# Kernel tuning notes

Measured on AMD Instinct MI355X. Metric: run time of the kernel, lower is better.

The kernel has to match this reference:

```python
import jax, jax.numpy as jnp
import numpy as np

HIDDEN, HEAD_DIM, B, S = 1024, 64, 8, 2048


def setup_inputs() -> dict:
    key = jax.random.key(0)
    ks = jax.random.split(key, 8)
    scale = 1.0 / np.sqrt(HIDDEN)
    return {
        "query": jax.random.normal(ks[0], (B, S, HIDDEN), jnp.float32),
        "key": jax.random.normal(ks[1], (B, S, HIDDEN), jnp.float32),
        "value": jax.random.normal(ks[2], (B, S, HIDDEN), jnp.float32),
        "relative_biases": jax.random.normal(ks[3], (B, S, S), jnp.float32),
        "mask": jnp.ones((B, S), jnp.int32),
        "Wq": jax.random.normal(ks[4], (HEAD_DIM, HIDDEN), jnp.float32) * scale,
        "bq": jnp.zeros((HEAD_DIM,), jnp.float32),
        "Wk": jax.random.normal(ks[5], (HEAD_DIM, HIDDEN), jnp.float32) * scale,
        "bk": jnp.zeros((HEAD_DIM,), jnp.float32),
        "Wv": jax.random.normal(ks[6], (HEAD_DIM, HIDDEN), jnp.float32) * scale,
        "bv": jnp.zeros((HEAD_DIM,), jnp.float32),
    }


def reference(query, key, value, relative_biases, mask, Wq, bq, Wk, bk, Wv, bv):
    # Per-head linear projections: [B,S,H] @ [H,D] + [D]
    q = jnp.einsum("bsh,dh->bsd", query, Wq) + bq
    k = jnp.einsum("bsh,dh->bsd", key, Wk) + bk
    v = jnp.einsum("bsh,dh->bsd", value, Wv) + bv
    d = q.shape[-1]
    # (QK^T + relative_bias) / sqrt(d)  -- bias added BEFORE scaling, as in source
    scores = (jnp.einsum("bqd,bkd->bqk", q, k) + relative_biases) / jnp.sqrt(
        jnp.asarray(d, q.dtype)
    )
    # 2-D mask [B,Sk] broadcast over queries; masked_fill(mask==0, -inf)
    m = mask[:, None, :]  # [B,1,Sk]
    scores = jnp.where(m == 0, -jnp.inf, scores)
    att = jax.nn.softmax(scores, axis=-1)
    # dropout prob 0.0 (eval / identity)
    return jnp.einsum("bqk,bkd->bqd", att, v)
```

## Files before the change

### kernel.cpp

```cpp
#include <hip/hip_runtime.h>
#include <stdint.h>

typedef __bf16 bf16x4 __attribute__((ext_vector_type(4)));
typedef __bf16 bf16x8 __attribute__((ext_vector_type(8)));
typedef float  f32x4  __attribute__((ext_vector_type(4)));

#define HID 1024
#define SEQ 2048
#define NB  8

__device__ __forceinline__ void gl_lds16(const void* g, void* l) {
    __builtin_amdgcn_global_load_lds(
        (const __attribute__((address_space(1))) void*)g,
        (__attribute__((address_space(3))) void*)l, 16, 0, 0);
}

__global__ __launch_bounds__(256) void prep_w(
    const float* __restrict__ Wq, const float* __restrict__ Wk,
    const float* __restrict__ Wv, __bf16* __restrict__ Wb)
{
    const int i = blockIdx.x * 256 + threadIdx.x;
    const int mat = i >> 14;
    const int j   = i & 16383;
    const float* src = ((mat == 0) ? Wq : (mat == 1) ? Wk : Wv) + j * 4;
    float4 f = *(const float4*)src;
    bf16x4 o = { (__bf16)f.x, (__bf16)f.y, (__bf16)f.z, (__bf16)f.w };
    *(bf16x4*)(Wb + (size_t)i * 4) = o;
}

__global__ __launch_bounds__(256, 3) void proj_kernel(
    const float* __restrict__ Xq, const float* __restrict__ Xk, const float* __restrict__ Xv,
    const __bf16* __restrict__ Wb,
    const float* __restrict__ bq_, const float* __restrict__ bk_, const float* __restrict__ bv_,
    __bf16* __restrict__ qo, __bf16* __restrict__ ko, __bf16* __restrict__ vTo)
{
    const int mat = blockIdx.y;
    const float* X   = (mat == 0) ? Xq  : (mat == 1) ? Xk  : Xv;
    const __bf16* Wm = Wb + (size_t)mat * 64 * HID;
    const float* Bp  = (mat == 0) ? bq_ : (mat == 1) ? bk_ : bv_;

    const int row0 = blockIdx.x * 64;
    const int tid  = threadIdx.x;
    const int lane = tid & 63;
    const int wv   = tid >> 6;
    const int lr   = lane & 15;
    const int g    = lane >> 4;

    __shared__ __align__(16) float  Xl[2][64 * 64];
    __shared__ __align__(16) __bf16 Wl[2][64 * 64];

    f32x4 acc[4] = {};

    auto STAGE = [&](int t, int pb) {
        const int k0 = t * 64;
        #pragma unroll
        for (int j = 0; j < 4; ++j) {
            const int row = wv * 16 + 4 * j + (lane >> 4);
            const int c   = row & 7;
            const float* src = X + (size_t)(row0 + row) * HID + k0 + 4 * ((lane & 15) ^ c);
            gl_lds16(src, &Xl[pb][(wv * 16 + 4 * j) * 64]);
        }
        #pragma unroll
        for (int j = 0; j < 2; ++j) {
            const int row = wv * 16 + 8 * j + (lane >> 3);
            const int c   = row & 7;
            const __bf16* src = Wm + (size_t)row * HID + k0 + 8 * ((lane & 7) ^ c);
            gl_lds16(src, &Wl[pb][(wv * 16 + 8 * j) * 64]);
        }
    };

    STAGE(0, 0);
    STAGE(1, 1);

    const int r  = wv * 16 + lr;
    const int cx = lr & 7;

    for (int t = 0; t < 16; ++t) {
        const int pb = t & 1;
        if (t < 15) { asm volatile("s_waitcnt vmcnt(6)" ::: "memory"); }
        else        { asm volatile("s_waitcnt vmcnt(0)" ::: "memory"); }
        __builtin_amdgcn_s_barrier();

        #pragma unroll
        for (int kk = 0; kk < 2; ++kk) {
            const int ulo = 2 * g + 8 * kk;
            f32x4 xa = *(const f32x4*)&Xl[pb][r * 64 + (((ulo)     ^ cx) << 2)];
            f32x4 xb = *(const f32x4*)&Xl[pb][r * 64 + (((ulo + 1) ^ cx) << 2)];
            bf16x8 af = { (__bf16)xa.x, (__bf16)xa.y, (__bf16)xa.z, (__bf16)xa.w,
                          (__bf16)xb.x, (__bf16)xb.y, (__bf16)xb.z, (__bf16)xb.w };
            #pragma unroll
            for (int ct = 0; ct < 4; ++ct) {
                const int uw = g + 4 * kk;
                bf16x8 bf = *(const bf16x8*)&Wl[pb][(ct * 16 + lr) * 64 + ((uw ^ cx) << 3)];
                acc[ct] = __builtin_amdgcn_mfma_f32_16x16x32_bf16(af, bf, acc[ct], 0, 0, 0);
            }
        }

        __builtin_amdgcn_s_barrier();
        if (t + 2 < 16) STAGE(t + 2, pb);
    }

    const float scl = (mat == 0) ? 0.125f : 1.0f;
    float res[4][4];
    #pragma unroll
    for (int ct = 0; ct < 4; ++ct) {
        const float bval = Bp[ct * 16 + lr];
        #pragma unroll
        for (int rr = 0; rr < 4; ++rr) res[ct][rr] = (acc[ct][rr] + bval) * scl;
    }

    if (mat < 2) {
        __bf16* o = (mat == 0) ? qo : ko;
        #pragma unroll
        for (int ct = 0; ct < 4; ++ct)
            #pragma unroll
            for (int rr = 0; rr < 4; ++rr)
                o[(size_t)(row0 + wv * 16 + 4 * g + rr) * 64 + ct * 16 + lr] = (__bf16)res[ct][rr];
    } else {
        __bf16* Tl = (__bf16*)&Xl[0][0];
        __syncthreads();
        #pragma unroll
        for (int ct = 0; ct < 4; ++ct)
            #pragma unroll
            for (int rr = 0; rr < 4; ++rr)
                Tl[(ct * 16 + lr) * 72 + wv * 16 + 4 * g + rr] = (__bf16)res[ct][rr];
        __syncthreads();
        const int d   = tid >> 2;
        const int sc_ = (tid & 3) * 16;
        const int b   = row0 >> 11;
        const int s0  = row0 & 2047;
        __bf16* dst = vTo + ((size_t)b * 64 + d) * SEQ + s0 + sc_;
        *(bf16x8*)dst       = *(const bf16x8*)&Tl[d * 72 + sc_];
        *(bf16x8*)(dst + 8) = *(const bf16x8*)&Tl[d * 72 + sc_ + 8];
    }
}

__global__ __launch_bounds__(128) void attn_kernel(
    const __bf16* __restrict__ qws, const __bf16* __restrict__ kws,
    const __bf16* __restrict__ vTws, const float* __restrict__ bias,
    const int* __restrict__ mask, float* __restrict__ out)
{
    const int bid = blockIdx.x;
    const int b   = bid & 7;
    const int q0  = (bid >> 3) * 32;
    const int tid = threadIdx.x;
    const int lane = tid & 63;
    const int wv   = tid >> 6;
    const int lr   = lane & 15;
    const int g    = lane >> 4;

    __shared__ __align__(16) __bf16 Kl[64 * 72];
    __shared__ __align__(16) __bf16 Vl[64 * 72];

    const int qrow = q0 + wv * 16 + lr;

    bf16x8 qf[2];
    {
        const __bf16* qp = qws + (size_t)(b * SEQ + qrow) * 64;
        #pragma unroll
        for (int dt = 0; dt < 2; ++dt) {
            bf16x4 lo = *(const bf16x4*)(qp + dt * 32 + 4 * g);
            bf16x4 hi = *(const bf16x4*)(qp + dt * 32 + 16 + 4 * g);
            qf[dt] = __builtin_shufflevector(lo, hi, 0, 1, 2, 3, 4, 5, 6, 7);
        }
    }

    f32x4 O[4] = {};
    float m   = -3.0e38f;
    float ell = 0.0f;

    const float* brow = bias + (size_t)(b * SEQ + qrow) * SEQ;
    const int*   mrow = mask + b * SEQ;

    const int sr = tid >> 1;
    const int sc = (tid & 1) * 32;
    const __bf16* kbase = kws  + (size_t)(b * SEQ + sr) * 64 + sc;
    const __bf16* vbase = vTws + ((size_t)b * 64 + sr) * SEQ + sc;

    bf16x8 kr[4], vr[4];
    float4 bvn[4]; int4 mkn[4];

    auto loadt = [&](int kt) {
        const __bf16* ks = kbase + (size_t)kt * 64;
        kr[0] = *(const bf16x8*)ks;
        kr[1] = *(const bf16x8*)(ks + 8);
        kr[2] = *(const bf16x8*)(ks + 16);
        kr[3] = *(const bf16x8*)(ks + 24);
        const __bf16* vs = vbase + kt;
        vr[0] = *(const bf16x8*)vs;
        vr[1] = *(const bf16x8*)(vs + 8);
        vr[2] = *(const bf16x8*)(vs + 16);
        vr[3] = *(const bf16x8*)(vs + 24);
        #pragma unroll
        for (int s2t = 0; s2t < 4; ++s2t) {
            bvn[s2t] = *(const float4*)(brow + kt + s2t * 16 + 4 * g);
            mkn[s2t] = *(const int4*)(mrow + kt + s2t * 16 + 4 * g);
        }
    };

    loadt(0);

    #pragma unroll 2
    for (int kt = 0; kt < SEQ; kt += 64) {
        *(bf16x8*)&Kl[sr * 72 + sc]      = kr[0];
        *(bf16x8*)&Kl[sr * 72 + sc + 8]  = kr[1];
        *(bf16x8*)&Kl[sr * 72 + sc + 16] = kr[2];
        *(bf16x8*)&Kl[sr * 72 + sc + 24] = kr[3];
        *(bf16x8*)&Vl[sr * 72 + sc]      = vr[0];
        *(bf16x8*)&Vl[sr * 72 + sc + 8]  = vr[1];
        *(bf16x8*)&Vl[sr * 72 + sc + 16] = vr[2];
        *(bf16x8*)&Vl[sr * 72 + sc + 24] = vr[3];
        float4 bv4[4]; int4 mk4[4];
        #pragma unroll
        for (int s2t = 0; s2t < 4; ++s2t) { bv4[s2t] = bvn[s2t]; mk4[s2t] = mkn[s2t]; }
        __syncthreads();

        if (kt + 64 < SEQ) loadt(kt + 64);

        float p[16];
        #pragma unroll
        for (int s2t = 0; s2t < 4; ++s2t) {
            const int s2 = s2t * 16;
            f32x4 acc = {};
            #pragma unroll
            for (int dt = 0; dt < 2; ++dt) {
                bf16x4 klo = *(const bf16x4*)&Kl[(s2 + lr) * 72 + dt * 32 + 4 * g];
                bf16x4 khi = *(const bf16x4*)&Kl[(s2 + lr) * 72 + dt * 32 + 16 + 4 * g];
                bf16x8 kf = __builtin_shufflevector(klo, khi, 0, 1, 2, 3, 4, 5, 6, 7);
                acc = __builtin_amdgcn_mfma_f32_16x16x32_bf16(kf, qf[dt], acc, 0, 0, 0);
            }
            p[s2t * 4 + 0] = mk4[s2t].x ? acc[0] + 0.125f * bv4[s2t].x : -1e30f;
            p[s2t * 4 + 1] = mk4[s2t].y ? acc[1] + 0.125f * bv4[s2t].y : -1e30f;
            p[s2t * 4 + 2] = mk4[s2t].z ? acc[2] + 0.125f * bv4[s2t].z : -1e30f;
            p[s2t * 4 + 3] = mk4[s2t].w ? acc[3] + 0.125f * bv4[s2t].w : -1e30f;
        }

        float tmax = p[0];
        #pragma unroll
        for (int i = 1; i < 16; ++i) tmax = fmaxf(tmax, p[i]);
        tmax = fmaxf(tmax, __shfl_xor(tmax, 16));
        tmax = fmaxf(tmax, __shfl_xor(tmax, 32));
        const float mnew  = fmaxf(m, tmax);
        const float scale = __expf(m - mnew);
        m = mnew;
        float ssum = 0.0f;
        #pragma unroll
        for (int i = 0; i < 16; ++i) { p[i] = __expf(p[i] - mnew); ssum += p[i]; }
        ssum += __shfl_xor(ssum, 16);
        ssum += __shfl_xor(ssum, 32);
        ell = ell * scale + ssum;

        float scr[4];
        #pragma unroll
        for (int rr = 0; rr < 4; ++rr) scr[rr] = __shfl(scale, 4 * g + rr);
        #pragma unroll
        for (int t = 0; t < 4; ++t)
            #pragma unroll
            for (int rr = 0; rr < 4; ++rr) O[t][rr] *= scr[rr];

        bf16x8 pf0 = { (__bf16)p[0],  (__bf16)p[1],  (__bf16)p[2],  (__bf16)p[3],
                       (__bf16)p[4],  (__bf16)p[5],  (__bf16)p[6],  (__bf16)p[7] };
        bf16x8 pf1 = { (__bf16)p[8],  (__bf16)p[9],  (__bf16)p[10], (__bf16)p[11],
                       (__bf16)p[12], (__bf16)p[13], (__bf16)p[14], (__bf16)p[15] };

        #pragma unroll
        for (int t = 0; t < 4; ++t) {
            const int dr = (t * 16 + lr) * 72;
            bf16x4 v0lo = *(const bf16x4*)&Vl[dr + 4 * g];
            bf16x4 v0hi = *(const bf16x4*)&Vl[dr + 16 + 4 * g];
            bf16x8 vf0 = __builtin_shufflevector(v0lo, v0hi, 0, 1, 2, 3, 4, 5, 6, 7);
            O[t] = __builtin_amdgcn_mfma_f32_16x16x32_bf16(pf0, vf0, O[t], 0, 0, 0);
            bf16x4 v1lo = *(const bf16x4*)&Vl[dr + 32 + 4 * g];
            bf16x4 v1hi = *(const bf16x4*)&Vl[dr + 48 + 4 * g];
            bf16x8 vf1 = __builtin_shufflevector(v1lo, v1hi, 0, 1, 2, 3, 4, 5, 6, 7);
            O[t] = __builtin_amdgcn_mfma_f32_16x16x32_bf16(pf1, vf1, O[t], 0, 0, 0);
        }
        __syncthreads();
    }

    float linv[4];
    #pragma unroll
    for (int rr = 0; rr < 4; ++rr) linv[rr] = 1.0f / __shfl(ell, 4 * g + rr);

    float* orow = out + (size_t)(b * SEQ + q0 + wv * 16) * 64;
    #pragma unroll
    for (int t = 0; t < 4; ++t)
        #pragma unroll
        for (int rr = 0; rr < 4; ++rr)
            orow[(size_t)(4 * g + rr) * 64 + t * 16 + lr] = O[t][rr] * linv[rr];
}

extern "C" void kernel_launch(void* const* d_in, const int* in_sizes, int n_in,
                              void* d_out, int out_size, void* d_ws, size_t ws_size,
                              hipStream_t stream) {
    const float* query = (const float*)d_in[0];
    const float* key_  = (const float*)d_in[1];
    const float* value = (const float*)d_in[2];
    const float* rb    = (const float*)d_in[3];
    const int*   mask  = (const int*)d_in[4];
    const float* Wq = (const float*)d_in[5];
    const float* bq = (const float*)d_in[6];
    const float* Wk = (const float*)d_in[7];
    const float* bk = (const float*)d_in[8];
    const float* Wv = (const float*)d_in[9];
    const float* bv = (const float*)d_in[10];

    __bf16* qws = (__bf16*)d_ws;
    __bf16* kws = qws + (size_t)16384 * 64;
    __bf16* vT  = kws + (size_t)16384 * 64;
    __bf16* Wb  = vT  + (size_t)8 * 64 * SEQ;

    hipLaunchKernelGGL(prep_w, dim3(192), dim3(256), 0, stream, Wq, Wk, Wv, Wb);
    hipLaunchKernelGGL(proj_kernel, dim3(256, 3), dim3(256), 0, stream,
                       query, key_, value, Wb, bq, bk, bv, qws, kws, vT);
    hipLaunchKernelGGL(attn_kernel, dim3(512), dim3(128), 0, stream,
                       qws, kws, vT, rb, mask, (float*)d_out);
}
```

Before: 97.29 us.

## Restructure projection kernel to register-staged loads with bf16 LDS and direct weight fragments

Replaces the async global-to-LDS staging of fp32 X and bf16 W tiles in the projection GEMM with register prefetch. X is loaded into registers, converted to bf16 once, and written to a smaller swizzled bf16 LDS buffer. Weight fragments are read directly from global into registers in MFMA layout, so there is no W LDS tile. The point is to cut LDS footprint and bandwidth and to hide load latency by software-pipelining the next tile's loads behind the current MFMAs. In exchange it needs more registers, drops the occupancy hint, and adds a full __syncthreads per tile.

```diff
diff --git a/kernel.cpp b/kernel.cpp
--- a/kernel.cpp
+++ b/kernel.cpp
@@ -8,12 +8,6 @@
 #define HID 1024
 #define SEQ 2048
 #define NB  8
-
-__device__ __forceinline__ void gl_lds16(const void* g, void* l) {
-    __builtin_amdgcn_global_load_lds(
-        (const __attribute__((address_space(1))) void*)g,
-        (__attribute__((address_space(3))) void*)l, 16, 0, 0);
-}
 
 __global__ __launch_bounds__(256) void prep_w(
     const float* __restrict__ Wq, const float* __restrict__ Wk,
@@ -28,7 +22,9 @@
     *(bf16x4*)(Wb + (size_t)i * 4) = o;
 }
 
-__global__ __launch_bounds__(256, 3) void proj_kernel(
+struct WFr { bf16x8 w[2][4]; };
+
+__global__ __launch_bounds__(256) void proj_kernel(
     const float* __restrict__ Xq, const float* __restrict__ Xk, const float* __restrict__ Xv,
     const __bf16* __restrict__ Wb,
     const float* __restrict__ bq_, const float* __restrict__ bk_, const float* __restrict__ bv_,
@@ -46,58 +42,61 @@
     const int lr   = lane & 15;
     const int g    = lane >> 4;
 
-    __shared__ __align__(16) float  Xl[2][64 * 64];
-    __shared__ __align__(16) __bf16 Wl[2][64 * 64];
+    __shared__ __align__(16) __bf16 Xl[2][64 * 64];
 
     f32x4 acc[4] = {};
-
-    auto STAGE = [&](int t, int pb) {
-        const int k0 = t * 64;
-        #pragma unroll
-        for (int j = 0; j < 4; ++j) {
-            const int row = wv * 16 + 4 * j + (lane >> 4);
-            const int c   = row & 7;
-            const float* src = X + (size_t)(row0 + row) * HID + k0 + 4 * ((lane & 15) ^ c);
-            gl_lds16(src, &Xl[pb][(wv * 16 + 4 * j) * 64]);
-        }
-        #pragma unroll
-        for (int j = 0; j < 2; ++j) {
-            const int row = wv * 16 + 8 * j + (lane >> 3);
-            const int c   = row & 7;
-            const __bf16* src = Wm + (size_t)row * HID + k0 + 8 * ((lane & 7) ^ c);
-            gl_lds16(src, &Wl[pb][(wv * 16 + 8 * j) * 64]);
-        }
-    };
-
-    STAGE(0, 0);
-    STAGE(1, 1);
-
-    const int r  = wv * 16 + lr;
-    const int cx = lr & 7;
-
-    for (int t = 0; t < 16; ++t) {
-        const int pb = t & 1;
-        if (t < 15) { asm volatile("s_waitcnt vmcnt(6)" ::: "memory"); }
-        else        { asm volatile("s_waitcnt vmcnt(0)" ::: "memory"); }
-        __builtin_amdgcn_s_barrier();
-
-        #pragma unroll
-        for (int kk = 0; kk < 2; ++kk) {
-            const int ulo = 2 * g + 8 * kk;
-            f32x4 xa = *(const f32x4*)&Xl[pb][r * 64 + (((ulo)     ^ cx) << 2)];
-            f32x4 xb = *(const f32x4*)&Xl[pb][r * 64 + (((ulo + 1) ^ cx) << 2)];
-            bf16x8 af = { (__bf16)xa.x, (__bf16)xa.y, (__bf16)xa.z, (__bf16)xa.w,
-                          (__bf16)xb.x, (__bf16)xb.y, (__bf16)xb.z, (__bf16)xb.w };
-            #pragma unroll
-            for (int ct = 0; ct < 4; ++ct) {
-                const int uw = g + 4 * kk;
-                bf16x8 bf = *(const bf16x8*)&Wl[pb][(ct * 16 + lr) * 64 + ((uw ^ cx) << 3)];
-                acc[ct] = __builtin_amdgcn_mfma_f32_16x16x32_bf16(af, bf, acc[ct], 0, 0, 0);
-            }
-        }
-
-        __builtin_amdgcn_s_barrier();
-        if (t + 2 < 16) STAGE(t + 2, pb);
+    float4 xr[4];
+    WFr Wa, Wb2;
+
+    auto LOADX = [&](int e) {
+        const int k0 = e * 64;
+        #pragma unroll
+        for (int i = 0; i < 4; ++i) {
+            const int row = wv * 16 + 4 * i + (lane >> 4);
+            xr[i] = *(const float4*)(X + (size_t)(row0 + row) * HID + k0 + (lane & 15) * 4);
+        }
+    };
+    auto LOADW = [&](WFr& W, int e) {
+        const int k0 = e * 64;
+        #pragma unroll
+        for (int s = 0; s < 2; ++s)
+            #pragma unroll
+            for (int ct = 0; ct < 4; ++ct)
+                W.w[s][ct] = *(const bf16x8*)(Wm + (size_t)(ct * 16 + lr) * HID + k0 + 32 * s + 8 * g);
+    };
+    auto WRITEX = [&](int pb) {
+        #pragma unroll
+        for (int i = 0; i < 4; ++i) {
+            const int row  = wv * 16 + 4 * i + (lane >> 4);
+            const int phys = (lane & 15) ^ ((row & 7) << 1);
+            bf16x4 v = { (__bf16)xr[i].x, (__bf16)xr[i].y, (__bf16)xr[i].z, (__bf16)xr[i].w };
+            *(bf16x4*)&Xl[pb][row * 64 + phys * 4] = v;
+        }
+    };
+    auto COMPUTE = [&](int pb, WFr& W) {
+        const int arow = wv * 16 + lr;
+        #pragma unroll
+        for (int s = 0; s < 2; ++s) {
+            const int phys = (8 * s + 2 * g) ^ ((lr & 7) << 1);
+            bf16x8 af = *(const bf16x8*)&Xl[pb][arow * 64 + phys * 4];
+            #pragma unroll
+            for (int ct = 0; ct < 4; ++ct)
+                acc[ct] = __builtin_amdgcn_mfma_f32_16x16x32_bf16(af, W.w[s][ct], acc[ct], 0, 0, 0);
+        }
+    };
+
+    LOADX(0); LOADW(Wa, 0);
+
+    #pragma unroll 1
+    for (int e = 0; e < 16; e += 2) {
+        WRITEX(0);
+        __syncthreads();
+        LOADX(e + 1); LOADW(Wb2, e + 1);
+        COMPUTE(0, Wa);
+        WRITEX(1);
+        __syncthreads();
+        if (e + 2 < 16) { LOADX(e + 2); LOADW(Wa, e + 2); }
+        COMPUTE(1, Wb2);
     }
 
     const float scl = (mat == 0) ? 0.125f : 1.0f;
@@ -117,7 +116,7 @@
             for (int rr = 0; rr < 4; ++rr)
                 o[(size_t)(row0 + wv * 16 + 4 * g + rr) * 64 + ct * 16 + lr] = (__bf16)res[ct][rr];
     } else {
-        __bf16* Tl = (__bf16*)&Xl[0][0];
+        __bf16* Tl = &Xl[0][0];
         __syncthreads();
         #pragma unroll
         for (int ct = 0; ct < 4; ++ct)
@@ -308,11 +307,11 @@
     __bf16* qws = (__bf16*)d_ws;
     __bf16* kws = qws + (size_t)16384 * 64;
     __bf16* vT  = kws + (size_t)16384 * 64;
-    __bf16* Wb  = vT  + (size_t)8 * 64 * SEQ;
-
-    hipLaunchKernelGGL(prep_w, dim3(192), dim3(256), 0, stream, Wq, Wk, Wv, Wb);
+    __bf16* Wbf = vT  + (size_t)8 * 64 * SEQ;
+
+    hipLaunchKernelGGL(prep_w, dim3(192), dim3(256), 0, stream, Wq, Wk, Wv, Wbf);
     hipLaunchKernelGGL(proj_kernel, dim3(256, 3), dim3(256), 0, stream,
-                       query, key_, value, Wb, bq, bk, bv, qws, kws, vT);
+                       query, key_, value, Wbf, bq, bk, bv, qws, kws, vT);
     hipLaunchKernelGGL(attn_kernel, dim3(512), dim3(128), 0, stream,
                        qws, kws, vT, rb, mask, (float*)d_out);
 }
```

New measurement: 117.5 us. +20.8%, slower.
